# Optimization experiments

Measured on AMD Instinct MI355X. Metric: run time of the kernel, lower is better.

The kernel has to match this reference:

```python
import jax, jax.numpy as jnp
import numpy as np

B, T, I, H = 64, 512, 512, 512

def setup_inputs() -> dict:
    key = jax.random.key(0)
    k1, k2, k3, k4, k5 = jax.random.split(key, 5)
    stdv = 1.0 / np.sqrt(H)
    return {
        "x": jax.random.normal(k1, (B, T, I), dtype=jnp.float32),
        "h0": jax.random.normal(k2, (B, H), dtype=jnp.float32),
        "U_i": jax.random.uniform(k3, (I, H), minval=-stdv, maxval=stdv, dtype=jnp.float32),
        "V_i": jax.random.uniform(k4, (H, H), minval=-stdv, maxval=stdv, dtype=jnp.float32),
        "b_i": jax.random.uniform(k5, (H,), minval=-stdv, maxval=stdv, dtype=jnp.float32),
    }

def reference(x, h0, U_i, V_i, b_i):
    # Precompute the input projection for all timesteps as one big GEMM: [B,T,H]
    xU = jnp.einsum("bti,ih->bth", x, U_i) + b_i
    # Sequential recurrence over time with lax.scan (time-major carry)
    def step(h, xU_t):
        h_new = jnp.tanh(xU_t + h @ V_i)  # [B,H]
        return h_new, h_new
    _, hs = jax.lax.scan(step, h0, jnp.swapaxes(xU, 0, 1))  # hs: [T,B,H]
    return jnp.swapaxes(hs, 0, 1)  # [B,T,H]
```

## Files before the change

### kernel.cpp

```cpp
#include <hip/hip_runtime.h>
#include <hip/hip_bf16.h>

#define Bsz 64
#define Tsz 512
#define Isz 512
#define Hsz 512

__global__ __launch_bounds__(256) void p1_gemm(const float* __restrict__ X,
                                               const float* __restrict__ U,
                                               const float* __restrict__ bias,
                                               float* __restrict__ out) {
  const int K = Isz, N = Hsz;
  __shared__ float As[32][128];
  __shared__ float Bs[32][64];
  const int MB = (Bsz * Tsz) / 128;
  int bm = blockIdx.x & (MB - 1);
  int bn = blockIdx.x >> 8;
  int t = threadIdx.x;
  int tx = t & 15, ty = t >> 4;

  float acc[8][4];
#pragma unroll
  for (int r = 0; r < 8; r++)
#pragma unroll
    for (int c = 0; c < 4; c++) acc[r][c] = 0.f;

  const float* Xb = X + (size_t)bm * 128 * K;
  const float* Ub = U + bn * 64;

  for (int k0 = 0; k0 < K; k0 += 32) {
    int ar = t >> 3, aq = t & 7;
#pragma unroll
    for (int i = 0; i < 4; i++) {
      int row = ar + 32 * i;
      float4 v = *(const float4*)&Xb[(size_t)row * K + k0 + 4 * aq];
      As[4 * aq + 0][row] = v.x;
      As[4 * aq + 1][row] = v.y;
      As[4 * aq + 2][row] = v.z;
      As[4 * aq + 3][row] = v.w;
    }
    int bkk = t >> 4, bq = t & 15;
#pragma unroll
    for (int i = 0; i < 2; i++) {
      int kk = bkk + 16 * i;
      *(float4*)&Bs[kk][4 * bq] = *(const float4*)&Ub[(size_t)(k0 + kk) * N + 4 * bq];
    }
    __syncthreads();
#pragma unroll
    for (int kk = 0; kk < 32; kk++) {
      float4 A0 = *(const float4*)&As[kk][ty * 8];
      float4 A1 = *(const float4*)&As[kk][ty * 8 + 4];
      float4 B0 = *(const float4*)&Bs[kk][tx * 4];
      float av[8] = {A0.x, A0.y, A0.z, A0.w, A1.x, A1.y, A1.z, A1.w};
      float bv[4] = {B0.x, B0.y, B0.z, B0.w};
#pragma unroll
      for (int r = 0; r < 8; r++)
#pragma unroll
        for (int c = 0; c < 4; c++) acc[r][c] += av[r] * bv[c];
    }
    __syncthreads();
  }

  float4 bias4 = *(const float4*)&bias[bn * 64 + tx * 4];
  float bb[4] = {bias4.x, bias4.y, bias4.z, bias4.w};
#pragma unroll
  for (int r = 0; r < 8; r++) {
    float4 o;
    o.x = acc[r][0] + bb[0];
    o.y = acc[r][1] + bb[1];
    o.z = acc[r][2] + bb[2];
    o.w = acc[r][3] + bb[3];
    *(float4*)&out[((size_t)bm * 128 + ty * 8 + r) * N + bn * 64 + tx * 4] = o;
  }
}

#define NGrp 32
#define BPGrp 8
#define CPB 64

__device__ __forceinline__ float ftanh(float x) {
  float ax = fabsf(x);
  float e = __expf(2.f * ax);
  float r = 1.f - 2.f / (e + 1.f);
  return copysignf(r, x);
}

template <int CTRL>
__device__ __forceinline__ float dppadd(float x) {
  int y = __builtin_amdgcn_update_dpp(0, __float_as_int(x), CTRL, 0xf, 0xf, true);
  return x + __int_as_float(y);
}
__device__ __forceinline__ float swz16add(float x) {
  return x + __int_as_float(
                 __builtin_amdgcn_ds_swizzle(__float_as_int(x), 0x401F));
}

__device__ __forceinline__ unsigned long long packha(float h, int tag) {
  return (unsigned long long)__float_as_uint(h) |
         ((unsigned long long)(unsigned)tag << 32);
}

__global__ __launch_bounds__(512, 2) void p2_rnn(
    const float* __restrict__ h0, const float* __restrict__ V,
    float* __restrict__ out, unsigned long long* __restrict__ atoms) {
  extern __shared__ float sm[];
  float4* __restrict__ Vl = (float4*)sm;
  float* __restrict__ hsm = sm + 32768;

  int bid = blockIdx.x;
  int g = bid & 31;
  int jb = bid >> 5;
  int t = threadIdx.x;
  int cq = t >> 5, ks = t & 31;

  for (int rep = 0; rep < 16; rep++) {
    int idx = rep * 512 + t;
    int k = idx >> 4, cg = idx & 15;
    float4 gv = *(const float4*)&V[(size_t)k * Hsz + CPB * jb + 4 * cg];
    Vl[k * 16 + (cg ^ ((k >> 4) & 15))] = gv;
  }
  {
    int k = t;
    int kw = (k & 15) >> 1, kse = k >> 4, e = k & 1;
    float2 hv;
    hv.x = h0[(size_t)(2 * g + 0) * Hsz + k];
    hv.y = h0[(size_t)(2 * g + 1) * Hsz + k];
    *(float2*)&hsm[kw * 128 + kse * 4 + 2 * e] = hv;
  }
  __syncthreads();

  const int cs = cq ^ (ks & 15);
  const float4* vp = &Vl[(ks << 8) + cs];
#define LOADV(i)                                                     \
  float4 tv##i = vp[(i) * 16];                                       \
  float v##i##x = tv##i.x, v##i##y = tv##i.y, v##i##z = tv##i.z,     \
        v##i##w = tv##i.w;
  LOADV(0) LOADV(1) LOADV(2) LOADV(3) LOADV(4) LOADV(5) LOADV(6) LOADV(7)
  LOADV(8) LOADV(9) LOADV(10) LOADV(11) LOADV(12) LOADV(13) LOADV(14) LOADV(15)
#undef LOADV
  asm volatile("" : "+v"(v0x), "+v"(v0y), "+v"(v0z), "+v"(v0w),
                    "+v"(v1x), "+v"(v1y), "+v"(v1z), "+v"(v1w),
                    "+v"(v2x), "+v"(v2y), "+v"(v2z), "+v"(v2w),
                    "+v"(v3x), "+v"(v3y), "+v"(v3z), "+v"(v3w));
  asm volatile("" : "+v"(v4x), "+v"(v4y), "+v"(v4z), "+v"(v4w),
                    "+v"(v5x), "+v"(v5y), "+v"(v5z), "+v"(v5w),
                    "+v"(v6x), "+v"(v6y), "+v"(v6z), "+v"(v6w),
                    "+v"(v7x), "+v"(v7y), "+v"(v7z), "+v"(v7w));
  asm volatile("" : "+v"(v8x), "+v"(v8y), "+v"(v8z), "+v"(v8w),
                    "+v"(v9x), "+v"(v9y), "+v"(v9z), "+v"(v9w),
                    "+v"(v10x), "+v"(v10y), "+v"(v10z), "+v"(v10w),
                    "+v"(v11x), "+v"(v11y), "+v"(v11z), "+v"(v11w));
  asm volatile("" : "+v"(v12x), "+v"(v12y), "+v"(v12z), "+v"(v12w),
                    "+v"(v13x), "+v"(v13y), "+v"(v13z), "+v"(v13w),
                    "+v"(v14x), "+v"(v14y), "+v"(v14z), "+v"(v14w),
                    "+v"(v15x), "+v"(v15y), "+v"(v15z), "+v"(v15w));

  bool own = (ks < 8);
  int ob = ks >> 2, jj = ks & 3;
  int col = CPB * jb + cq * 4 + jj;
  size_t obase = ((size_t)(2 * g + ob) * Tsz) * Hsz + col;
  float xu = own ? out[obase] : 0.f;

  const int ks4 = ks * 4;
  const int pk = t;
  const int hwidx = ((pk & 15) >> 1) * 128 + (pk >> 4) * 4 + 2 * (pk & 1);

  for (int s = 0; s < Tsz; s++) {
    float xun = 0.f;
    if (own && s + 1 < Tsz) xun = out[obase + (size_t)(s + 1) * Hsz];

    const float* hp = &hsm[(s & 1) * 1024 + ks4];

    float aA0 = 0, aA1 = 0, aA2 = 0, aA3 = 0;
    float aB0 = 0, aB1 = 0, aB2 = 0, aB3 = 0;
#define STEPK(kp, a, b)                                                        \
  {                                                                            \
    float4 h4 = *(const float4*)&hp[(kp) * 128];                               \
    aA0 += v##a##x * h4.x + v##b##x * h4.z;                                    \
    aB0 += v##a##x * h4.y + v##b##x * h4.w;                                    \
    aA1 += v##a##y * h4.x + v##b##y * h4.z;                                    \
    aB1 += v##a##y * h4.y + v##b##y * h4.w;                                    \
    aA2 += v##a##z * h4.x + v##b##z * h4.z;                                    \
    aB2 += v##a##z * h4.y + v##b##z * h4.w;                                    \
    aA3 += v##a##w * h4.x + v##b##w * h4.z;                                    \
    aB3 += v##a##w * h4.y + v##b##w * h4.w;                                    \
  }
    STEPK(0, 0, 1)  STEPK(1, 2, 3)   STEPK(2, 4, 5)   STEPK(3, 6, 7)
    STEPK(4, 8, 9)  STEPK(5, 10, 11) STEPK(6, 12, 13) STEPK(7, 14, 15)
#undef STEPK

#define RED(x)                 \
  x = dppadd<0xB1>(x);         \
  x = dppadd<0x4E>(x);         \
  x = dppadd<0x124>(x);        \
  x = dppadd<0x128>(x);        \
  x = swz16add(x);
    RED(aA0) RED(aA1) RED(aA2) RED(aA3) RED(aB0) RED(aB1) RED(aB2) RED(aB3)
#undef RED

    int p = (s + 1) & 1;
    if (own) {
      float sum = ob ? ((jj & 2) ? ((jj & 1) ? aB3 : aB2) : ((jj & 1) ? aB1 : aB0))
                     : ((jj & 2) ? ((jj & 1) ? aA3 : aA2) : ((jj & 1) ? aA1 : aA0));
      float hv = ftanh(sum + xu);
      out[obase + (size_t)s * Hsz] = hv;
      if (s + 1 < Tsz)
        __hip_atomic_store(&atoms[((size_t)p * Bsz + 2 * g + ob) * Hsz + col],
                           packha(hv, s + 1), __ATOMIC_RELAXED,
                           __HIP_MEMORY_SCOPE_AGENT);
      xu = xun;
    }

    if (s + 1 < Tsz) {
      unsigned long long* q0 = &atoms[((size_t)p * Bsz + 2 * g + 0) * Hsz + pk];
      unsigned long long* q1 = &atoms[((size_t)p * Bsz + 2 * g + 1) * Hsz + pk];
      int want = s + 1;
      float hv0 = 0.f, hv1 = 0.f;
      bool d0 = false, d1 = false;
      int guard = 0;
      while (true) {
        if (!d0) {
          unsigned long long a = __hip_atomic_load(q0, __ATOMIC_RELAXED,
                                                   __HIP_MEMORY_SCOPE_AGENT);
          if ((int)(a >> 32) == want) { hv0 = __uint_as_float((unsigned)a); d0 = true; }
        }
        if (!d1) {
          unsigned long long a = __hip_atomic_load(q1, __ATOMIC_RELAXED,
                                                   __HIP_MEMORY_SCOPE_AGENT);
          if ((int)(a >> 32) == want) { hv1 = __uint_as_float((unsigned)a); d1 = true; }
        }
        if (d0 && d1) break;
        if (++guard > (1 << 20)) break;
      }
      float2 hv; hv.x = hv0; hv.y = hv1;
      *(float2*)&hsm[p * 1024 + hwidx] = hv;
      __syncthreads();
    }
  }
}

extern "C" void kernel_launch(void* const* d_in, const int* in_sizes, int n_in,
                              void* d_out, int out_size, void* d_ws, size_t ws_size,
                              hipStream_t stream) {
  const float* x  = (const float*)d_in[0];
  const float* h0 = (const float*)d_in[1];
  const float* U  = (const float*)d_in[2];
  const float* V  = (const float*)d_in[3];
  const float* b  = (const float*)d_in[4];
  float* out = (float*)d_out;
  unsigned long long* atoms = (unsigned long long*)d_ws;

  static const int kDynLds = (32768 + 2 * 1024) * 4;
  (void)hipFuncSetAttribute(reinterpret_cast<const void*>(p2_rnn),
                            hipFuncAttributeMaxDynamicSharedMemorySize, kDynLds);

  p1_gemm<<<dim3(2048), dim3(256), 0, stream>>>(x, U, b, out);

  p2_rnn<<<dim3(256), dim3(512), kDynLds, stream>>>(h0, V, out, atoms);
}
```

Measured before the change: 1.316 ms.

## Split recurrence into two staggered batch halves to overlap compute with polling

Each block previously computed both batch rows together and then waited for both rows' next hidden states from other blocks. The step is now split into two phases: row A is computed and published, then row B's hidden state is polled, then row B is computed while row A's next state is being produced elsewhere. The goal is to hide cross-block latency by letting one row's compute overlap the other row's communication. In exchange there are two barriers per step instead of one, and the LDS layout for h changes to per-row buffers.

After: 1.560 ms. 18.5% more time.

```diff
diff --git a/kernel.cpp b/kernel.cpp
--- a/kernel.cpp
+++ b/kernel.cpp
@@ -100,12 +100,23 @@
          ((unsigned long long)(unsigned)tag << 32);
 }
 
+__device__ __forceinline__ float poll_one(unsigned long long* q, int want) {
+  int guard = 0;
+  while (true) {
+    unsigned long long a =
+        __hip_atomic_load(q, __ATOMIC_RELAXED, __HIP_MEMORY_SCOPE_AGENT);
+    if ((int)(a >> 32) == want || ++guard > (1 << 20))
+      return __uint_as_float((unsigned)a);
+  }
+}
+
 __global__ __launch_bounds__(512, 2) void p2_rnn(
     const float* __restrict__ h0, const float* __restrict__ V,
     float* __restrict__ out, unsigned long long* __restrict__ atoms) {
   extern __shared__ float sm[];
   float4* __restrict__ Vl = (float4*)sm;
-  float* __restrict__ hsm = sm + 32768;
+  float* __restrict__ hA = sm + 32768;
+  float* __restrict__ hB = sm + 32768 + 1024;
 
   int bid = blockIdx.x;
   int g = bid & 31;
@@ -119,14 +130,9 @@
     float4 gv = *(const float4*)&V[(size_t)k * Hsz + CPB * jb + 4 * cg];
     Vl[k * 16 + (cg ^ ((k >> 4) & 15))] = gv;
   }
-  {
-    int k = t;
-    int kw = (k & 15) >> 1, kse = k >> 4, e = k & 1;
-    float2 hv;
-    hv.x = h0[(size_t)(2 * g + 0) * Hsz + k];
-    hv.y = h0[(size_t)(2 * g + 1) * Hsz + k];
-    *(float2*)&hsm[kw * 128 + kse * 4 + 2 * e] = hv;
-  }
+  const int islot = ((t & 15) >> 1) * 64 + 2 * (t >> 4) + (t & 1);
+  hA[islot] = h0[(size_t)(2 * g + 0) * Hsz + t];
+  hB[islot] = h0[(size_t)(2 * g + 1) * Hsz + t];
   __syncthreads();
 
   const int cs = cq ^ (ks & 15);
@@ -155,88 +161,90 @@
                     "+v"(v14x), "+v"(v14y), "+v"(v14z), "+v"(v14w),
                     "+v"(v15x), "+v"(v15y), "+v"(v15z), "+v"(v15w));
 
-  bool own = (ks < 8);
-  int ob = ks >> 2, jj = ks & 3;
-  int col = CPB * jb + cq * 4 + jj;
-  size_t obase = ((size_t)(2 * g + ob) * Tsz) * Hsz + col;
-  float xu = own ? out[obase] : 0.f;
-
-  const int ks4 = ks * 4;
+  const bool own = (ks < 4);
+  const int jj = ks & 3;
+  const int col = CPB * jb + cq * 4 + jj;
+  const size_t obA = ((size_t)(2 * g + 0) * Tsz) * Hsz + col;
+  const size_t obB = ((size_t)(2 * g + 1) * Tsz) * Hsz + col;
+  float xuA = own ? out[obA] : 0.f;
+  float xuB = own ? out[obB] : 0.f;
+
+  const int hb2 = 2 * ks;
   const int pk = t;
-  const int hwidx = ((pk & 15) >> 1) * 128 + (pk >> 4) * 4 + 2 * (pk & 1);
-
-  for (int s = 0; s < Tsz; s++) {
-    float xun = 0.f;
-    if (own && s + 1 < Tsz) xun = out[obase + (size_t)(s + 1) * Hsz];
-
-    const float* hp = &hsm[(s & 1) * 1024 + ks4];
-
-    float aA0 = 0, aA1 = 0, aA2 = 0, aA3 = 0;
-    float aB0 = 0, aB1 = 0, aB2 = 0, aB3 = 0;
-#define STEPK(kp, a, b)                                                        \
-  {                                                                            \
-    float4 h4 = *(const float4*)&hp[(kp) * 128];                               \
-    aA0 += v##a##x * h4.x + v##b##x * h4.z;                                    \
-    aB0 += v##a##x * h4.y + v##b##x * h4.w;                                    \
-    aA1 += v##a##y * h4.x + v##b##y * h4.z;                                    \
-    aB1 += v##a##y * h4.y + v##b##y * h4.w;                                    \
-    aA2 += v##a##z * h4.x + v##b##z * h4.z;                                    \
-    aB2 += v##a##z * h4.y + v##b##z * h4.w;                                    \
-    aA3 += v##a##w * h4.x + v##b##w * h4.z;                                    \
-    aB3 += v##a##w * h4.y + v##b##w * h4.w;                                    \
-  }
-    STEPK(0, 0, 1)  STEPK(1, 2, 3)   STEPK(2, 4, 5)   STEPK(3, 6, 7)
-    STEPK(4, 8, 9)  STEPK(5, 10, 11) STEPK(6, 12, 13) STEPK(7, 14, 15)
-#undef STEPK
-
+
+#define PK2(H, kp, a, b, A0, A1, A2, A3)              \
+  {                                                   \
+    float2 h2 = *(const float2*)&(H)[(kp) * 64];      \
+    A0 += v##a##x * h2.x + v##b##x * h2.y;            \
+    A1 += v##a##y * h2.x + v##b##y * h2.y;            \
+    A2 += v##a##z * h2.x + v##b##z * h2.y;            \
+    A3 += v##a##w * h2.x + v##b##w * h2.y;            \
+  }
+#define PIPE_FMA(H, A0, A1, A2, A3)                                        \
+  PK2(H, 0, 0, 1, A0, A1, A2, A3) PK2(H, 1, 2, 3, A0, A1, A2, A3)          \
+  PK2(H, 2, 4, 5, A0, A1, A2, A3) PK2(H, 3, 6, 7, A0, A1, A2, A3)          \
+  PK2(H, 4, 8, 9, A0, A1, A2, A3) PK2(H, 5, 10, 11, A0, A1, A2, A3)        \
+  PK2(H, 6, 12, 13, A0, A1, A2, A3) PK2(H, 7, 14, 15, A0, A1, A2, A3)
 #define RED(x)                 \
   x = dppadd<0xB1>(x);         \
   x = dppadd<0x4E>(x);         \
   x = dppadd<0x124>(x);        \
   x = dppadd<0x128>(x);        \
   x = swz16add(x);
-    RED(aA0) RED(aA1) RED(aA2) RED(aA3) RED(aB0) RED(aB1) RED(aB2) RED(aB3)
+
+  for (int s = 0; s < Tsz; s++) {
+    const int par = s & 1, pn = (s + 1) & 1;
+
+    float xan = (own && s + 1 < Tsz) ? out[obA + (size_t)(s + 1) * Hsz] : 0.f;
+    {
+      const float* hp = &hA[par * 512 + hb2];
+      float a0 = 0.f, a1 = 0.f, a2 = 0.f, a3 = 0.f;
+      PIPE_FMA(hp, a0, a1, a2, a3)
+      RED(a0) RED(a1) RED(a2) RED(a3)
+      if (own) {
+        float sum = (jj & 2) ? ((jj & 1) ? a3 : a2) : ((jj & 1) ? a1 : a0);
+        float hv = ftanh(sum + xuA);
+        out[obA + (size_t)s * Hsz] = hv;
+        if (s + 1 < Tsz)
+          __hip_atomic_store(&atoms[((size_t)pn * Bsz + 2 * g + 0) * Hsz + col],
+                             packha(hv, s + 1), __ATOMIC_RELAXED,
+                             __HIP_MEMORY_SCOPE_AGENT);
+        xuA = xan;
+      }
+    }
+    if (s > 0) {
+      float hv = poll_one(&atoms[((size_t)par * Bsz + 2 * g + 1) * Hsz + pk], s);
+      hB[par * 512 + islot] = hv;
+    }
+    __syncthreads();
+
+    float xbn = (own && s + 1 < Tsz) ? out[obB + (size_t)(s + 1) * Hsz] : 0.f;
+    {
+      const float* hq = &hB[par * 512 + hb2];
+      float b0 = 0.f, b1 = 0.f, b2 = 0.f, b3 = 0.f;
+      PIPE_FMA(hq, b0, b1, b2, b3)
+      RED(b0) RED(b1) RED(b2) RED(b3)
+      if (own) {
+        float sum = (jj & 2) ? ((jj & 1) ? b3 : b2) : ((jj & 1) ? b1 : b0);
+        float hv = ftanh(sum + xuB);
+        out[obB + (size_t)s * Hsz] = hv;
+        if (s + 1 < Tsz)
+          __hip_atomic_store(&atoms[((size_t)pn * Bsz + 2 * g + 1) * Hsz + col],
+                             packha(hv, s + 1), __ATOMIC_RELAXED,
+                             __HIP_MEMORY_SCOPE_AGENT);
+        xuB = xbn;
+      }
+    }
+    if (s + 1 < Tsz) {
+      float hv =
+          poll_one(&atoms[((size_t)pn * Bsz + 2 * g + 0) * Hsz + pk], s + 1);
+      hA[pn * 512 + islot] = hv;
+    }
+    __syncthreads();
+  }
+#undef PK2
+#undef PIPE_FMA
 #undef RED
-
-    int p = (s + 1) & 1;
-    if (own) {
-      float sum = ob ? ((jj & 2) ? ((jj & 1) ? aB3 : aB2) : ((jj & 1) ? aB1 : aB0))
-                     : ((jj & 2) ? ((jj & 1) ? aA3 : aA2) : ((jj & 1) ? aA1 : aA0));
-      float hv = ftanh(sum + xu);
-      out[obase + (size_t)s * Hsz] = hv;
-      if (s + 1 < Tsz)
-        __hip_atomic_store(&atoms[((size_t)p * Bsz + 2 * g + ob) * Hsz + col],
-                           packha(hv, s + 1), __ATOMIC_RELAXED,
-                           __HIP_MEMORY_SCOPE_AGENT);
-      xu = xun;
-    }
-
-    if (s + 1 < Tsz) {
-      unsigned long long* q0 = &atoms[((size_t)p * Bsz + 2 * g + 0) * Hsz + pk];
-      unsigned long long* q1 = &atoms[((size_t)p * Bsz + 2 * g + 1) * Hsz + pk];
-      int want = s + 1;
-      float hv0 = 0.f, hv1 = 0.f;
-      bool d0 = false, d1 = false;
-      int guard = 0;
-      while (true) {
-        if (!d0) {
-          unsigned long long a = __hip_atomic_load(q0, __ATOMIC_RELAXED,
-                                                   __HIP_MEMORY_SCOPE_AGENT);
-          if ((int)(a >> 32) == want) { hv0 = __uint_as_float((unsigned)a); d0 = true; }
-        }
-        if (!d1) {
-          unsigned long long a = __hip_atomic_load(q1, __ATOMIC_RELAXED,
-                                                   __HIP_MEMORY_SCOPE_AGENT);
-          if ((int)(a >> 32) == want) { hv1 = __uint_as_float((unsigned)a); d1 = true; }
-        }
-        if (d0 && d1) break;
-        if (++guard > (1 << 20)) break;
-      }
-      float2 hv; hv.x = hv0; hv.y = hv1;
-      *(float2*)&hsm[p * 1024 + hwidx] = hv;
-      __syncthreads();
-    }
-  }
 }
 
 extern "C" void kernel_launch(void* const* d_in, const int* in_sizes, int n_in,
```
